# Optimization experiments

Measured on AMD Instinct MI355X. Metric: run time of the kernel, lower is better.

## Reference

```python
import jax, jax.numpy as jnp
import numpy as np

TOP_K = 4
B, S, H, E, F = 2, 2048, 2048, 32, 768


def setup_inputs() -> dict:
    key = jax.random.key(0)
    k0, k1, k2, k3, k4 = jax.random.split(key, 5)
    scale = 0.02
    return {
        "hidden_states": jax.random.normal(k0, (B, S, H), jnp.float32),
        "gate_w": jax.random.normal(k1, (E, H), jnp.float32) * scale,   # router Linear weight [out,in]
        "w_gate": jax.random.normal(k2, (E, H, F), jnp.float32) * scale,  # gate_proj per expert
        "w_up": jax.random.normal(k3, (E, H, F), jnp.float32) * scale,    # up_proj per expert
        "w_down": jax.random.normal(k4, (E, F, H), jnp.float32) * scale,  # down_proj per expert
    }


def reference(hidden_states, gate_w, w_gate, w_up, w_down):
    b, s, h = hidden_states.shape
    x = hidden_states.reshape(-1, h)                      # [T, H]
    T = x.shape[0]
    n_exp = gate_w.shape[0]

    # Router: logits -> float32 softmax -> top-k -> renormalize (norm_topk_prob)
    router_logits = x @ gate_w.T                          # [T, E]
    probs = jax.nn.softmax(router_logits.astype(jnp.float32), axis=-1)
    top_w, top_i = jax.lax.top_k(probs, TOP_K)            # [T, K]
    top_w = top_w / jnp.sum(top_w, axis=-1, keepdims=True)
    top_w = top_w.astype(x.dtype)

    # Dense combine matrix [T, E]: routing weight for selected experts, 0 elsewhere
    combine = jnp.zeros((T, n_exp), x.dtype).at[
        jnp.arange(T)[:, None], top_i
    ].add(top_w)

    # Scan over experts: SwiGLU MLP, weighted accumulate. Keeps peak mem ~ T*F.
    def step(acc, ws):
        wg, wu, wd, cw = ws                               # [H,F],[H,F],[F,H],[T]
        hdn = jax.nn.silu(x @ wg) * (x @ wu)              # [T, F]
        return acc + cw[:, None] * (hdn @ wd), None

    out, _ = jax.lax.scan(
        step, jnp.zeros((T, h), x.dtype), (w_gate, w_up, w_down, combine.T)
    )
    return out.reshape(b, s, h), router_logits
```

## Files before the change

kernel.cpp:

```cpp
#include <hip/hip_runtime.h>
#include <hip/hip_bf16.h>

#define T_TOK 4096
#define HID 2048
#define NE 32
#define FF 768
#define TOPK 4
#define NSLOT (T_TOK * TOPK)

typedef __bf16 bf16;
typedef __bf16 bf16x4 __attribute__((ext_vector_type(4)));
typedef __bf16 bf16x8 __attribute__((ext_vector_type(8)));
typedef float f32x4 __attribute__((ext_vector_type(4)));

__device__ __forceinline__ void async_copy16(const void* g, void* l) {
    __builtin_amdgcn_global_load_lds(
        (const __attribute__((address_space(1))) void*)g,
        (__attribute__((address_space(3))) void*)l, 16, 0, 0);
}

__device__ __forceinline__ void fence_barrier() {
    __builtin_amdgcn_s_barrier();
    asm volatile("" ::: "memory");
}

__global__ __launch_bounds__(256) void transpose_cvt_kernel(
    const float* __restrict__ in, bf16* __restrict__ outp, int R, int C)
{
    const size_t mo = (size_t)blockIdx.z * R * C;
    const float* A = in + mo;
    bf16* O = outp + mo;
    const int c0 = blockIdx.x * 64;
    const int r0 = blockIdx.y * 64;
    __shared__ bf16 T[64][72];
    const int tid = threadIdx.x;
    const int rr = tid >> 4;
    const int cc = (tid & 15) * 4;
#pragma unroll
    for (int p = 0; p < 4; ++p) {
        int r = p * 16 + rr;
        float4 v = *(const float4*)(A + (size_t)(r0 + r) * C + c0 + cc);
        bf16x4 b = {(bf16)v.x, (bf16)v.y, (bf16)v.z, (bf16)v.w};
        *(bf16x4*)&T[r][cc] = b;
    }
    __syncthreads();
    const int c = tid >> 3;
    const int rb = (tid & 7) * 8;
#pragma unroll
    for (int p = 0; p < 2; ++p) {
        int cw = p * 32 + c;
        bf16 tmp[8] __attribute__((aligned(16)));
#pragma unroll
        for (int j = 0; j < 8; ++j) tmp[j] = T[rb + j][cw];
        *(bf16x8*)(O + (size_t)(c0 + cw) * R + r0 + rb) = *(bf16x8*)tmp;
    }
}

__global__ __launch_bounds__(256) void router_kernel(
    const float* __restrict__ x, const float* __restrict__ gw,
    float* __restrict__ logits_out, int* __restrict__ topi,
    float* __restrict__ topw, int* __restrict__ counts, bf16* __restrict__ xb)
{
    const int t = blockIdx.x;
    __shared__ float xs[HID];
    __shared__ float lg[NE];
    __shared__ float ps[NE];
    const float4* xr = (const float4*)(x + (size_t)t * HID);
    float4* xs4 = (float4*)xs;
    for (int i = threadIdx.x; i < HID / 4; i += 256) xs4[i] = xr[i];
    __syncthreads();

    {
        const float4* xsp = (const float4*)xs + threadIdx.x * 2;
        float4 a = xsp[0], b = xsp[1];
        bf16x8 v = {(bf16)a.x, (bf16)a.y, (bf16)a.z, (bf16)a.w,
                    (bf16)b.x, (bf16)b.y, (bf16)b.z, (bf16)b.w};
        *(bf16x8*)(xb + (size_t)t * HID + threadIdx.x * 8) = v;
    }

    const int e = threadIdx.x >> 3;
    const int part = threadIdx.x & 7;
    const float4* gr = (const float4*)(gw + (size_t)e * HID + part * 256);
    const float4* xp = (const float4*)(xs + part * 256);
    float sum = 0.f;
#pragma unroll 8
    for (int i = 0; i < 64; ++i) {
        float4 g = gr[i], v = xp[i];
        sum += g.x * v.x + g.y * v.y + g.z * v.z + g.w * v.w;
    }
    sum += __shfl_down(sum, 4, 8);
    sum += __shfl_down(sum, 2, 8);
    sum += __shfl_down(sum, 1, 8);
    if (part == 0) { lg[e] = sum; logits_out[(size_t)t * NE + e] = sum; }
    __syncthreads();

    if (threadIdx.x == 0) {
        float mx = lg[0];
        for (int i = 1; i < NE; ++i) mx = fmaxf(mx, lg[i]);
        for (int i = 0; i < NE; ++i) ps[i] = __expf(lg[i] - mx);
        float tw[TOPK]; int ti[TOPK]; float ts = 0.f;
        for (int k = 0; k < TOPK; ++k) {
            float best = -1.f; int bi = 0;
            for (int i = 0; i < NE; ++i)
                if (ps[i] > best) { best = ps[i]; bi = i; }
            tw[k] = best; ti[k] = bi; ps[bi] = -2.f; ts += best;
        }
        const float inv = 1.f / ts;
        for (int k = 0; k < TOPK; ++k) {
            topi[t * TOPK + k] = ti[k];
            topw[t * TOPK + k] = tw[k] * inv;
            atomicAdd(&counts[ti[k]], 1);
        }
    }
}

__global__ void offsets_kernel(const int* __restrict__ counts,
                               int* __restrict__ offs, int* __restrict__ cursors)
{
    if (threadIdx.x == 0) {
        int acc = 0;
        for (int e2 = 0; e2 < NE; ++e2) { offs[e2] = acc; acc += counts[e2]; cursors[e2] = 0; }
    }
}

__global__ __launch_bounds__(256) void scatter_kernel(
    const int* __restrict__ topi, const float* __restrict__ topw,
    const int* __restrict__ offs, int* __restrict__ cursors,
    int* __restrict__ slot_token, float* __restrict__ slot_w)
{
    int t = blockIdx.x * 256 + threadIdx.x;
    if (t >= T_TOK) return;
#pragma unroll
    for (int k = 0; k < TOPK; ++k) {
        int e2 = topi[t * TOPK + k];
        int pos = atomicAdd(&cursors[e2], 1);
        int idx = offs[e2] + pos;
        slot_token[idx] = t;
        slot_w[idx] = topw[t * TOPK + k];
    }
}

__global__ __launch_bounds__(256) void gemm_gu2_kernel(
    const bf16* __restrict__ xb, const bf16* __restrict__ WTg,
    const bf16* __restrict__ WTu,
    const int* __restrict__ slot_token, const int* __restrict__ offs,
    const int* __restrict__ counts, bf16* __restrict__ GU, int nt_off)
{
    const int nt = blockIdx.x + nt_off;
    const int mt = blockIdx.y;
    const int e  = blockIdx.z;
    const int cnt = counts[e];
    if (mt * 128 >= cnt) return;
    const int off = offs[e];
    const bf16* W = (nt < 6) ? WTg : WTu;
    const bf16* B = W + (size_t)e * FF * HID + (size_t)((nt % 6) * 128) * HID;

    __shared__ __attribute__((aligned(16))) bf16 As[2][8192];
    __shared__ __attribute__((aligned(16))) bf16 Bs[2][8192];
    __shared__ int toks[128];

    const int tid = threadIdx.x;
    if (tid < 128) {
        int row = mt * 128 + tid;
        toks[tid] = slot_token[off + (row < cnt ? row : cnt - 1)];
    }
    __syncthreads();

    const int srow = tid >> 3;
    const int c_lds = tid & 7;
    const bf16* aptr[4];
    const bf16* bptr[4];
#pragma unroll
    for (int q = 0; q < 4; ++q) {
        int row = q * 32 + srow;
        int cg = c_lds ^ (row & 7);
        aptr[q] = xb + (size_t)toks[row] * HID + cg * 8;
        bptr[q] = B + (size_t)row * HID + cg * 8;
    }

    const int lane = tid & 63;
    const int w  = tid >> 6;
    const int wm = (w & 1) * 64;
    const int wn = (w >> 1) * 64;
    const int fr = lane & 15;
    const int kq = lane >> 4;

    f32x4 acc[4][4];
#pragma unroll
    for (int i = 0; i < 4; ++i)
#pragma unroll
        for (int j = 0; j < 4; ++j) acc[i][j] = {0.f, 0.f, 0.f, 0.f};

#pragma unroll
    for (int q = 0; q < 4; ++q) async_copy16(aptr[q], &As[0][q * 2048 + tid * 8]);
#pragma unroll
    for (int q = 0; q < 4; ++q) async_copy16(bptr[q], &Bs[0][q * 2048 + tid * 8]);

    int cur = 0;
    for (int kk = 0; kk < HID; kk += 64) {
        if (kk + 64 < HID) {
            const int nb = cur ^ 1;
#pragma unroll
            for (int q = 0; q < 4; ++q) async_copy16(aptr[q] + kk + 64, &As[nb][q * 2048 + tid * 8]);
#pragma unroll
            for (int q = 0; q < 4; ++q) async_copy16(bptr[q] + kk + 64, &Bs[nb][q * 2048 + tid * 8]);
            asm volatile("s_waitcnt vmcnt(8)" ::: "memory");
        } else {
            asm volatile("s_waitcnt vmcnt(0)" ::: "memory");
        }
        fence_barrier();
        const bf16* Ab = As[cur];
        const bf16* Bb = Bs[cur];
#pragma unroll
        for (int ks = 0; ks < 2; ++ks) {
            bf16x8 a[4], b[4];
#pragma unroll
            for (int i = 0; i < 4; ++i) {
                int row = wm + i * 16 + fr;
                int ch = (ks * 4 + kq) ^ (row & 7);
                a[i] = *(const bf16x8*)(Ab + row * 64 + ch * 8);
            }
#pragma unroll
            for (int j = 0; j < 4; ++j) {
                int n = wn + j * 16 + fr;
                int ch = (ks * 4 + kq) ^ (n & 7);
                b[j] = *(const bf16x8*)(Bb + n * 64 + ch * 8);
            }
#pragma unroll
            for (int i = 0; i < 4; ++i)
#pragma unroll
                for (int j = 0; j < 4; ++j)
                    acc[i][j] = __builtin_amdgcn_mfma_f32_16x16x32_bf16(a[i], b[j], acc[i][j], 0, 0, 0);
        }
        asm volatile("s_waitcnt lgkmcnt(0)" ::: "memory");
        fence_barrier();
        cur ^= 1;
    }

    const int colBase = nt * 128 + wn;
#pragma unroll
    for (int i = 0; i < 4; ++i) {
#pragma unroll
        for (int r = 0; r < 4; ++r) {
            int mloc = wm + i * 16 + kq * 4 + r;
            int row = mt * 128 + mloc;
            if (row < cnt) {
                bf16* dst = GU + (size_t)(off + row) * (2 * FF) + colBase;
#pragma unroll
                for (int j = 0; j < 4; ++j)
                    dst[j * 16 + fr] = (bf16)acc[i][j][r];
            }
        }
    }
}

__global__ __launch_bounds__(256) void silu_mul_kernel(
    const bf16* __restrict__ GU, bf16* __restrict__ hdn)
{
    size_t idx = ((size_t)blockIdx.x * 256 + threadIdx.x) * 8;
    size_t s = idx / FF;
    int f = (int)(idx % FF);
    const bf16* gp = GU + s * (2 * FF) + f;
    bf16x8 g8 = *(const bf16x8*)gp;
    bf16x8 u8 = *(const bf16x8*)(gp + FF);
    bf16x8 o;
#pragma unroll
    for (int i = 0; i < 8; ++i) {
        float g = (float)g8[i], u = (float)u8[i];
        float sl = g / (1.f + __expf(-g));
        o[i] = (bf16)(sl * u);
    }
    *(bf16x8*)(hdn + s * FF + f) = o;
}

__global__ __launch_bounds__(256) void gemm_down2_kernel(
    const bf16* __restrict__ hdn, const bf16* __restrict__ WT,
    const int* __restrict__ slot_token, const float* __restrict__ slot_w,
    const int* __restrict__ offs, const int* __restrict__ counts,
    float* __restrict__ out)
{
    const int nt = blockIdx.x;
    const int mt = blockIdx.y;
    const int e  = blockIdx.z;
    const int cnt = counts[e];
    if (mt * 128 >= cnt) return;
    const int off = offs[e];
    const bf16* B = WT + (size_t)e * HID * FF + (size_t)(nt * 128) * FF;

    __shared__ __attribute__((aligned(16))) bf16 As[2][8192];
    __shared__ __attribute__((aligned(16))) bf16 Bs[2][8192];
    __shared__ int toks[128];
    __shared__ float wts[128];

    const int tid = threadIdx.x;
    if (tid < 128) {
        int row = mt * 128 + tid;
        if (row < cnt) { toks[tid] = slot_token[off + row]; wts[tid] = slot_w[off + row]; }
        else           { toks[tid] = 0; wts[tid] = 0.f; }
    }
    __syncthreads();

    const int srow = tid >> 3;
    const int c_lds = tid & 7;
    const bf16* aptr[4];
    const bf16* bptr[4];
#pragma unroll
    for (int q = 0; q < 4; ++q) {
        int row = q * 32 + srow;
        int cg = c_lds ^ (row & 7);
        int sl = off + mt * 128 + row;
        if (sl > NSLOT - 1) sl = NSLOT - 1;
        aptr[q] = hdn + (size_t)sl * FF + cg * 8;
        bptr[q] = B + (size_t)row * FF + cg * 8;
    }

    const int lane = tid & 63;
    const int w  = tid >> 6;
    const int wm = (w & 1) * 64;
    const int wn = (w >> 1) * 64;
    const int fr = lane & 15;
    const int kq = lane >> 4;

    f32x4 acc[4][4];
#pragma unroll
    for (int i = 0; i < 4; ++i)
#pragma unroll
        for (int j = 0; j < 4; ++j) acc[i][j] = {0.f, 0.f, 0.f, 0.f};

#pragma unroll
    for (int q = 0; q < 4; ++q) async_copy16(aptr[q], &As[0][q * 2048 + tid * 8]);
#pragma unroll
    for (int q = 0; q < 4; ++q) async_copy16(bptr[q], &Bs[0][q * 2048 + tid * 8]);

    int cur = 0;
    for (int kk = 0; kk < FF; kk += 64) {
        if (kk + 64 < FF) {
            const int nb = cur ^ 1;
#pragma unroll
            for (int q = 0; q < 4; ++q) async_copy16(aptr[q] + kk + 64, &As[nb][q * 2048 + tid * 8]);
#pragma unroll
            for (int q = 0; q < 4; ++q) async_copy16(bptr[q] + kk + 64, &Bs[nb][q * 2048 + tid * 8]);
            asm volatile("s_waitcnt vmcnt(8)" ::: "memory");
        } else {
            asm volatile("s_waitcnt vmcnt(0)" ::: "memory");
        }
        fence_barrier();
        const bf16* Ab = As[cur];
        const bf16* Bb = Bs[cur];
#pragma unroll
        for (int ks = 0; ks < 2; ++ks) {
            bf16x8 a[4], b[4];
#pragma unroll
            for (int i = 0; i < 4; ++i) {
                int row = wm + i * 16 + fr;
                int ch = (ks * 4 + kq) ^ (row & 7);
                a[i] = *(const bf16x8*)(Ab + row * 64 + ch * 8);
            }
#pragma unroll
            for (int j = 0; j < 4; ++j) {
                int n = wn + j * 16 + fr;
                int ch = (ks * 4 + kq) ^ (n & 7);
                b[j] = *(const bf16x8*)(Bb + n * 64 + ch * 8);
            }
#pragma unroll
            for (int i = 0; i < 4; ++i)
#pragma unroll
                for (int j = 0; j < 4; ++j)
                    acc[i][j] = __builtin_amdgcn_mfma_f32_16x16x32_bf16(a[i], b[j], acc[i][j], 0, 0, 0);
        }
        asm volatile("s_waitcnt lgkmcnt(0)" ::: "memory");
        fence_barrier();
        cur ^= 1;
    }

    const int colBase = nt * 128 + wn;
#pragma unroll
    for (int i = 0; i < 4; ++i) {
#pragma unroll
        for (int r = 0; r < 4; ++r) {
            int mloc = wm + i * 16 + kq * 4 + r;
            int row = mt * 128 + mloc;
            if (row < cnt) {
                int tok = toks[mloc];
                float wgt = wts[mloc];
                float* dst = out + (size_t)tok * HID + colBase;
#pragma unroll
                for (int j = 0; j < 4; ++j)
                    atomicAdd(&dst[j * 16 + fr], acc[i][j][r] * wgt);
            }
        }
    }
}

extern "C" void kernel_launch(void* const* d_in, const int* in_sizes, int n_in,
                              void* d_out, int out_size, void* d_ws, size_t ws_size,
                              hipStream_t stream)
{
    const float* x  = (const float*)d_in[0];
    const float* gw = (const float*)d_in[1];
    const float* wg = (const float*)d_in[2];
    const float* wu = (const float*)d_in[3];
    const float* wd = (const float*)d_in[4];
    float* out    = (float*)d_out;
    float* logits = out + (size_t)T_TOK * HID;

    char* ws = (char*)d_ws;
    size_t o = 0;
    bf16* xb  = (bf16*)(ws + o); o += (size_t)T_TOK * HID * 2;
    bf16* GU  = (bf16*)(ws + o); o += (size_t)NSLOT * 1536 * 2;
    bf16* hdn = (bf16*)(ws + o); o += (size_t)NSLOT * 768 * 2;
    int*   topi = (int*)(ws + o);        o += (size_t)T_TOK * TOPK * 4;
    float* topw = (float*)(ws + o);      o += (size_t)T_TOK * TOPK * 4;
    int*   slot_token = (int*)(ws + o);  o += (size_t)T_TOK * TOPK * 4;
    float* slot_w = (float*)(ws + o);    o += (size_t)T_TOK * TOPK * 4;
    int* counts  = (int*)(ws + o);
    int* offs    = counts + 32;
    int* cursors = counts + 64;
    o += 256;
    const size_t Welems = (size_t)NE * HID * FF;
    bf16* WTg = (bf16*)(ws + o);
    const bool big = ws_size >= o + 3 * Welems * sizeof(bf16);
    bf16* WTu = big ? WTg + Welems : WTg;
    bf16* WTd = big ? WTu + Welems : WTg;

    hipMemsetAsync(out, 0, (size_t)T_TOK * HID * sizeof(float), stream);
    hipMemsetAsync(counts, 0, 32 * sizeof(int), stream);

    router_kernel<<<T_TOK, 256, 0, stream>>>(x, gw, logits, topi, topw, counts, xb);
    offsets_kernel<<<1, 64, 0, stream>>>(counts, offs, cursors);
    scatter_kernel<<<T_TOK / 256, 256, 0, stream>>>(topi, topw, offs, cursors, slot_token, slot_w);

    if (big) {
        transpose_cvt_kernel<<<dim3(FF / 64, HID / 64, NE), 256, 0, stream>>>(wg, WTg, HID, FF);
        transpose_cvt_kernel<<<dim3(FF / 64, HID / 64, NE), 256, 0, stream>>>(wu, WTu, HID, FF);
        transpose_cvt_kernel<<<dim3(HID / 64, FF / 64, NE), 256, 0, stream>>>(wd, WTd, FF, HID);
        gemm_gu2_kernel<<<dim3(12, 32, NE), 256, 0, stream>>>(xb, WTg, WTu, slot_token, offs, counts, GU, 0);
        silu_mul_kernel<<<(NSLOT * FF / 8) / 256, 256, 0, stream>>>(GU, hdn);
        gemm_down2_kernel<<<dim3(16, 32, NE), 256, 0, stream>>>(hdn, WTd, slot_token, slot_w, offs, counts, out);
    } else {
        transpose_cvt_kernel<<<dim3(FF / 64, HID / 64, NE), 256, 0, stream>>>(wg, WTg, HID, FF);
        gemm_gu2_kernel<<<dim3(6, 32, NE), 256, 0, stream>>>(xb, WTg, WTg, slot_token, offs, counts, GU, 0);
        transpose_cvt_kernel<<<dim3(FF / 64, HID / 64, NE), 256, 0, stream>>>(wu, WTg, HID, FF);
        gemm_gu2_kernel<<<dim3(6, 32, NE), 256, 0, stream>>>(xb, WTg, WTg, slot_token, offs, counts, GU, 6);
        silu_mul_kernel<<<(NSLOT * FF / 8) / 256, 256, 0, stream>>>(GU, hdn);
        transpose_cvt_kernel<<<dim3(HID / 64, FF / 64, NE), 256, 0, stream>>>(wd, WTg, FF, HID);
        gemm_down2_kernel<<<dim3(16, 32, NE), 256, 0, stream>>>(hdn, WTg, slot_token, slot_w, offs, counts, out);
    }
}
```

Measured before the change: 1.081 ms.

## Replace down-proj fp32 atomic scatter with per-slot bf16 output and gather combine

The down-projection GEMM no longer atomically adds weighted fp32 results into the token-major output. It now writes plain bf16 rows per routed slot into a buffer that reuses the dead gate-weight workspace. A new combine kernel gathers each token's TOPK slot rows via a slot_of map, weights them and writes the output directly, which also drops the output memset. The weight transpose/convert kernel is reworked to pack bf16 pairs and do wider stores. This trades global atomics for an extra 64MB bf16 round trip, and rounds the expert outputs to bf16 before combining.

Result: faster. 1.047 ms (-3.1%).

```diff
diff --git a/kernel.cpp b/kernel.cpp
--- a/kernel.cpp
+++ b/kernel.cpp
@@ -9,6 +9,7 @@
 #define NSLOT (T_TOK * TOPK)
 
 typedef __bf16 bf16;
+typedef __bf16 bf16x2 __attribute__((ext_vector_type(2)));
 typedef __bf16 bf16x4 __attribute__((ext_vector_type(4)));
 typedef __bf16 bf16x8 __attribute__((ext_vector_type(8)));
 typedef float f32x4 __attribute__((ext_vector_type(4)));
@@ -32,28 +33,32 @@
     bf16* O = outp + mo;
     const int c0 = blockIdx.x * 64;
     const int r0 = blockIdx.y * 64;
-    __shared__ bf16 T[64][72];
+    __shared__ bf16 Tt[64][66];
     const int tid = threadIdx.x;
-    const int rr = tid >> 4;
-    const int cc = (tid & 15) * 4;
-#pragma unroll
-    for (int p = 0; p < 4; ++p) {
-        int r = p * 16 + rr;
-        float4 v = *(const float4*)(A + (size_t)(r0 + r) * C + c0 + cc);
-        bf16x4 b = {(bf16)v.x, (bf16)v.y, (bf16)v.z, (bf16)v.w};
-        *(bf16x4*)&T[r][cc] = b;
+    const int p = tid >> 3;
+    const int g = tid & 7;
+    const float* ap = A + (size_t)(r0 + 2 * p) * C + c0 + g * 8;
+    float4 a0 = *(const float4*)(ap);
+    float4 a1 = *(const float4*)(ap + 4);
+    float4 b0 = *(const float4*)(ap + C);
+    float4 b1 = *(const float4*)(ap + C + 4);
+    float va[8] = {a0.x, a0.y, a0.z, a0.w, a1.x, a1.y, a1.z, a1.w};
+    float vb[8] = {b0.x, b0.y, b0.z, b0.w, b1.x, b1.y, b1.z, b1.w};
+#pragma unroll
+    for (int i = 0; i < 8; ++i) {
+        bf16x2 v = {(bf16)va[i], (bf16)vb[i]};
+        *(bf16x2*)&Tt[g * 8 + i][2 * p] = v;
     }
     __syncthreads();
-    const int c = tid >> 3;
-    const int rb = (tid & 7) * 8;
-#pragma unroll
-    for (int p = 0; p < 2; ++p) {
-        int cw = p * 32 + c;
-        bf16 tmp[8] __attribute__((aligned(16)));
-#pragma unroll
-        for (int j = 0; j < 8; ++j) tmp[j] = T[rb + j][cw];
-        *(bf16x8*)(O + (size_t)(c0 + cw) * R + r0 + rb) = *(bf16x8*)tmp;
-    }
+    const int c = tid >> 2;
+    const int rb = (tid & 3) * 16;
+    bf16 tmp[16] __attribute__((aligned(16)));
+#pragma unroll
+    for (int j = 0; j < 8; ++j)
+        *(bf16x2*)&tmp[2 * j] = *(const bf16x2*)&Tt[c][rb + 2 * j];
+    bf16* dst = O + (size_t)(c0 + c) * R + r0 + rb;
+    *(bf16x8*)dst = *(bf16x8*)tmp;
+    *(bf16x8*)(dst + 8) = *(bf16x8*)(tmp + 8);
 }
 
 __global__ __launch_bounds__(256) void router_kernel(
@@ -126,7 +131,7 @@
 __global__ __launch_bounds__(256) void scatter_kernel(
     const int* __restrict__ topi, const float* __restrict__ topw,
     const int* __restrict__ offs, int* __restrict__ cursors,
-    int* __restrict__ slot_token, float* __restrict__ slot_w)
+    int* __restrict__ slot_token, int* __restrict__ slot_of)
 {
     int t = blockIdx.x * 256 + threadIdx.x;
     if (t >= T_TOK) return;
@@ -136,7 +141,7 @@
         int pos = atomicAdd(&cursors[e2], 1);
         int idx = offs[e2] + pos;
         slot_token[idx] = t;
-        slot_w[idx] = topw[t * TOPK + k];
+        slot_of[t * TOPK + k] = idx;
     }
 }
 
@@ -275,9 +280,8 @@
 
 __global__ __launch_bounds__(256) void gemm_down2_kernel(
     const bf16* __restrict__ hdn, const bf16* __restrict__ WT,
-    const int* __restrict__ slot_token, const float* __restrict__ slot_w,
     const int* __restrict__ offs, const int* __restrict__ counts,
-    float* __restrict__ out)
+    bf16* __restrict__ dslot)
 {
     const int nt = blockIdx.x;
     const int mt = blockIdx.y;
@@ -289,17 +293,8 @@
 
     __shared__ __attribute__((aligned(16))) bf16 As[2][8192];
     __shared__ __attribute__((aligned(16))) bf16 Bs[2][8192];
-    __shared__ int toks[128];
-    __shared__ float wts[128];
 
     const int tid = threadIdx.x;
-    if (tid < 128) {
-        int row = mt * 128 + tid;
-        if (row < cnt) { toks[tid] = slot_token[off + row]; wts[tid] = slot_w[off + row]; }
-        else           { toks[tid] = 0; wts[tid] = 0.f; }
-    }
-    __syncthreads();
-
     const int srow = tid >> 3;
     const int c_lds = tid & 7;
     const bf16* aptr[4];
@@ -381,15 +376,43 @@
             int mloc = wm + i * 16 + kq * 4 + r;
             int row = mt * 128 + mloc;
             if (row < cnt) {
-                int tok = toks[mloc];
-                float wgt = wts[mloc];
-                float* dst = out + (size_t)tok * HID + colBase;
+                bf16* dst = dslot + (size_t)(off + row) * HID + colBase;
 #pragma unroll
                 for (int j = 0; j < 4; ++j)
-                    atomicAdd(&dst[j * 16 + fr], acc[i][j][r] * wgt);
-            }
-        }
-    }
+                    dst[j * 16 + fr] = (bf16)acc[i][j][r];
+            }
+        }
+    }
+}
+
+__global__ __launch_bounds__(256) void combine_kernel(
+    const bf16* __restrict__ dslot, const int* __restrict__ slot_of,
+    const float* __restrict__ topw, float* __restrict__ out)
+{
+    const int t = blockIdx.x;
+    __shared__ int sl[TOPK];
+    __shared__ float sw[TOPK];
+    if (threadIdx.x < TOPK) {
+        sl[threadIdx.x] = slot_of[t * TOPK + threadIdx.x];
+        sw[threadIdx.x] = topw[t * TOPK + threadIdx.x];
+    }
+    __syncthreads();
+    const int h = threadIdx.x * 8;
+    float acc[8];
+#pragma unroll
+    for (int i = 0; i < 8; ++i) acc[i] = 0.f;
+#pragma unroll
+    for (int k = 0; k < TOPK; ++k) {
+        bf16x8 v = *(const bf16x8*)(dslot + (size_t)sl[k] * HID + h);
+        float wk = sw[k];
+#pragma unroll
+        for (int i = 0; i < 8; ++i) acc[i] += wk * (float)v[i];
+    }
+    float4* dst = (float4*)(out + (size_t)t * HID + h);
+    float4 o0 = {acc[0], acc[1], acc[2], acc[3]};
+    float4 o1 = {acc[4], acc[5], acc[6], acc[7]};
+    dst[0] = o0;
+    dst[1] = o1;
 }
 
 extern "C" void kernel_launch(void* const* d_in, const int* in_sizes, int n_in,
@@ -412,23 +435,24 @@
     int*   topi = (int*)(ws + o);        o += (size_t)T_TOK * TOPK * 4;
     float* topw = (float*)(ws + o);      o += (size_t)T_TOK * TOPK * 4;
     int*   slot_token = (int*)(ws + o);  o += (size_t)T_TOK * TOPK * 4;
-    float* slot_w = (float*)(ws + o);    o += (size_t)T_TOK * TOPK * 4;
+    int*   slot_of = (int*)(ws + o);     o += (size_t)T_TOK * TOPK * 4;
     int* counts  = (int*)(ws + o);
     int* offs    = counts + 32;
     int* cursors = counts + 64;
     o += 256;
     const size_t Welems = (size_t)NE * HID * FF;
+    const size_t Wbytes = Welems * sizeof(bf16);
     bf16* WTg = (bf16*)(ws + o);
-    const bool big = ws_size >= o + 3 * Welems * sizeof(bf16);
+    const bool big = ws_size >= o + 3 * Wbytes;
     bf16* WTu = big ? WTg + Welems : WTg;
     bf16* WTd = big ? WTu + Welems : WTg;
-
-    hipMemsetAsync(out, 0, (size_t)T_TOK * HID * sizeof(float), stream);
+    bf16* dslot = big ? WTg : (bf16*)((char*)WTg + Wbytes);
+
     hipMemsetAsync(counts, 0, 32 * sizeof(int), stream);
 
     router_kernel<<<T_TOK, 256, 0, stream>>>(x, gw, logits, topi, topw, counts, xb);
     offsets_kernel<<<1, 64, 0, stream>>>(counts, offs, cursors);
-    scatter_kernel<<<T_TOK / 256, 256, 0, stream>>>(topi, topw, offs, cursors, slot_token, slot_w);
+    scatter_kernel<<<T_TOK / 256, 256, 0, stream>>>(topi, topw, offs, cursors, slot_token, slot_of);
 
     if (big) {
         transpose_cvt_kernel<<<dim3(FF / 64, HID / 64, NE), 256, 0, stream>>>(wg, WTg, HID, FF);
@@ -436,7 +460,7 @@
         transpose_cvt_kernel<<<dim3(HID / 64, FF / 64, NE), 256, 0, stream>>>(wd, WTd, FF, HID);
         gemm_gu2_kernel<<<dim3(12, 32, NE), 256, 0, stream>>>(xb, WTg, WTu, slot_token, offs, counts, GU, 0);
         silu_mul_kernel<<<(NSLOT * FF / 8) / 256, 256, 0, stream>>>(GU, hdn);
-        gemm_down2_kernel<<<dim3(16, 32, NE), 256, 0, stream>>>(hdn, WTd, slot_token, slot_w, offs, counts, out);
+        gemm_down2_kernel<<<dim3(16, 32, NE), 256, 0, stream>>>(hdn, WTd, offs, counts, dslot);
     } else {
         transpose_cvt_kernel<<<dim3(FF / 64, HID / 64, NE), 256, 0, stream>>>(wg, WTg, HID, FF);
         gemm_gu2_kernel<<<dim3(6, 32, NE), 256, 0, stream>>>(xb, WTg, WTg, slot_token, offs, counts, GU, 0);
@@ -444,6 +468,7 @@
         gemm_gu2_kernel<<<dim3(6, 32, NE), 256, 0, stream>>>(xb, WTg, WTg, slot_token, offs, counts, GU, 6);
         silu_mul_kernel<<<(NSLOT * FF / 8) / 256, 256, 0, stream>>>(GU, hdn);
         transpose_cvt_kernel<<<dim3(HID / 64, FF / 64, NE), 256, 0, stream>>>(wd, WTg, FF, HID);
-        gemm_down2_kernel<<<dim3(16, 32, NE), 256, 0, stream>>>(hdn, WTg, slot_token, slot_w, offs, counts, out);
-    }
-}
+        gemm_down2_kernel<<<dim3(16, 32, NE), 256, 0, stream>>>(hdn, WTg, offs, counts, dslot);
+    }
+    combine_kernel<<<T_TOK, 256, 0, stream>>>(dslot, slot_of, topw, out);
+}
```
